# Performance work log

Hardware: AMD Instinct MI355X
Metric: run time of the kernel (lower is better)

The kernel has to match this reference:

```python
import jax, jax.numpy as jnp
import numpy as np

DIM = 1024
BLOCK = 64
N_BLOCKS = DIM // BLOCK
N = 65536
INIT_SCALE = 0.01


def setup_inputs() -> dict:
    key = jax.random.key(0)
    k1, k2 = jax.random.split(key)
    x = jax.random.normal(k1, (N, DIM), dtype=jnp.float32)
    skew_params = jax.random.normal(k2, (N_BLOCKS, BLOCK, BLOCK), dtype=jnp.float32) * INIT_SCALE
    perm = jnp.asarray(np.random.default_rng(0).permutation(DIM), dtype=jnp.int64)
    return {"x": x, "skew_params": skew_params, "perm": perm}


def reference(x, skew_params, perm):
    # Skew-symmetrize each block: A = P - P^T, shape [K, b, b]
    A = skew_params - jnp.swapaxes(skew_params, -1, -2)
    # Per-block orthogonal matrices via matrix exponential, [K, b, b]
    B = jax.vmap(jax.scipy.linalg.expm)(A)
    # Block-diagonal matmul without materializing the dense [dim, dim] matrix:
    # x @ block_diag(B_0..B_{K-1}) == batched per-block matmul on reshaped x.
    xb = x.reshape(x.shape[0], N_BLOCKS, BLOCK)          # [N, K, b]
    yb = jnp.einsum("nkb,kbc->nkc", xb, B)               # [N, K, b]
    y = yb.reshape(x.shape[0], DIM)                      # [N, dim]
    # Shuffle: column permutation
    return y[:, perm]
```

## Files before the change

kernel.cpp:

```cpp
#include <hip/hip_runtime.h>

#define DIM           1024
#define BLK           64
#define NB            16
#define RT            16
#define MAIN_THREADS  1024
#define NWG           256
#define TPW           16
#define P68           68
#define BFRAG_STRIDE  512

typedef float  f32x4  __attribute__((ext_vector_type(4)));
typedef unsigned uintx2 __attribute__((ext_vector_type(2)));
typedef short  bf16x8 __attribute__((ext_vector_type(8)));

static __device__ __forceinline__ ushort f2bf(float f) {
    union { float f; unsigned u; } v; v.f = f;
    unsigned r = v.u + 0x7fffu + ((v.u >> 16) & 1u);
    return (ushort)(r >> 16);
}
static __device__ __forceinline__ float bfhi2f(unsigned hi_bits) {
    union { unsigned u; float f; } v; v.u = hi_bits & 0xffff0000u; return v.f;
}
static __device__ __forceinline__ float bflo2f(unsigned lo_bits) {
    union { unsigned u; float f; } v; v.u = lo_bits << 16; return v.f;
}

#define WAITL()   asm volatile("s_waitcnt lgkmcnt(0)" ::: "memory")
#define SBAR()    __builtin_amdgcn_s_barrier()

__global__ __launch_bounds__(512) void expm_kernel(
        const float* __restrict__ skew, ushort* __restrict__ Btl,
        const int* __restrict__ praw, int* __restrict__ pinv) {
    __shared__ float Asm[BLK][P68];
    __shared__ float Tb[2][BLK][P68];
    __shared__ float Rm[BLK][P68];
    const int tid = threadIdx.x;

    if (blockIdx.x == NB) {
        __shared__ int zc;
        if (tid == 0) zc = 0;
        __syncthreads();
        int local = 0;
        for (int i = tid; i < DIM; i += 512)
            if (praw[i] == 0) local++;
        if (local) atomicAdd(&zc, local);
        __syncthreads();
        const bool is64 = (zc > 100);
        const long long* p64 = (const long long*)praw;
        for (int i = tid; i < DIM; i += 512) {
            const int v = is64 ? (int)p64[i] : praw[i];
            pinv[v] = i;
        }
        return;
    }

    const int k = blockIdx.x;
    const float* P = skew + (size_t)k * (BLK * BLK);

    for (int e = tid; e < BLK * BLK; e += 512) {
        const int i = e >> 6, j = e & 63;
        const float a = P[i * BLK + j] - P[j * BLK + i];
        Asm[i][j]   = a;
        Tb[0][i][j] = a;
        Rm[i][j]    = a + (i == j ? 1.0f : 0.0f);
    }
    __syncthreads();

    const int i0 = (tid >> 4) * 2;
    const int j0 = (tid & 15) * 4;

    for (int n = 2; n <= 7; ++n) {
        const float invn = 1.0f / (float)n;
        const float (*Tc)[P68] = Tb[n & 1];
        float       (*Tn)[P68] = Tb[1 - (n & 1)];
        f32x4 acc0 = {0.f, 0.f, 0.f, 0.f}, acc1 = {0.f, 0.f, 0.f, 0.f};
        for (int b = 0; b < BLK; ++b) {
            const f32x4 av = *(const f32x4*)&Asm[b][j0];
            acc0 += Tc[i0][b]     * av;
            acc1 += Tc[i0 + 1][b] * av;
        }
        acc0 *= invn; acc1 *= invn;
        *(f32x4*)&Tn[i0][j0]     = acc0;
        *(f32x4*)&Tn[i0 + 1][j0] = acc1;
        f32x4 r0 = *(const f32x4*)&Rm[i0][j0];     r0 += acc0; *(f32x4*)&Rm[i0][j0]     = r0;
        f32x4 r1 = *(const f32x4*)&Rm[i0 + 1][j0]; r1 += acc1; *(f32x4*)&Rm[i0 + 1][j0] = r1;
        __syncthreads();
    }

    for (int e = tid; e < BLK * BLK; e += 512) {
        const int b = e >> 6, c = e & 63;
        const int n = c >> 4, m = c & 15;
        const int h = b >> 5, g = (b >> 3) & 3, j = b & 7;
        const size_t idx = (size_t)((k * 4 + n) * 2 + h) * BFRAG_STRIDE
                         + g * 128 + m * 8 + j;
        Btl[idx] = (ushort)f2bf(Rm[b][c]);
    }
}

__global__ __launch_bounds__(MAIN_THREADS) void gsl_main_kernel(
        const float* __restrict__ x, const ushort* __restrict__ Btl,
        const int* __restrict__ pinv, float* __restrict__ out) {
    __shared__ ushort ybuf[2][RT * DIM];

    const int tid  = threadIdx.x;
    const int lane = tid & 63;
    const int w    = tid >> 6;
    const int g    = lane >> 4;
    const int m16  = lane & 15;

    bf16x8 bfr[4][2];
#pragma unroll
    for (int n = 0; n < 4; ++n)
#pragma unroll
        for (int h = 0; h < 2; ++h)
            bfr[n][h] = *(const bf16x8*)(Btl +
                (size_t)((w * 4 + n) * 2 + h) * BFRAG_STRIDE + lane * 8);

    int jb[4];
#pragma unroll
    for (int n = 0; n < 4; ++n)
        jb[n] = pinv[w * 64 + n * 16 + m16] * 2;

    const int tile0 = blockIdx.x * TPW;
    const float* xw = x + w * 64 + g * 8;

    const int rp   = w & 7;
    const int hh   = w >> 3;
    const int q32  = lane & 31;
    const int erow = 2 * rp + (lane >> 5);
    const int ecol = hh * 512 + q32 * 4;

    f32x4 a0, a1, a2, a3;
    {
        const float* xp = xw + (size_t)(tile0 * RT + m16) * DIM;
        a0 = *(const f32x4*)(xp);      a1 = *(const f32x4*)(xp + 4);
        a2 = *(const f32x4*)(xp + 32); a3 = *(const f32x4*)(xp + 36);
    }

    for (int it = 0; it < TPW; ++it) {
        char* const yc = (char*)ybuf[it & 1];

        bf16x8 alo, ahi;
        alo[0] = f2bf(a0[0]); alo[1] = f2bf(a0[1]); alo[2] = f2bf(a0[2]); alo[3] = f2bf(a0[3]);
        alo[4] = f2bf(a1[0]); alo[5] = f2bf(a1[1]); alo[6] = f2bf(a1[2]); alo[7] = f2bf(a1[3]);
        ahi[0] = f2bf(a2[0]); ahi[1] = f2bf(a2[1]); ahi[2] = f2bf(a2[2]); ahi[3] = f2bf(a2[3]);
        ahi[4] = f2bf(a3[0]); ahi[5] = f2bf(a3[1]); ahi[6] = f2bf(a3[2]); ahi[7] = f2bf(a3[3]);

        if (it + 1 < TPW) {
            const float* xp = xw + (size_t)((tile0 + it + 1) * RT + m16) * DIM;
            a0 = *(const f32x4*)(xp);      a1 = *(const f32x4*)(xp + 4);
            a2 = *(const f32x4*)(xp + 32); a3 = *(const f32x4*)(xp + 36);
        }

        f32x4 acc[4];
#pragma unroll
        for (int n = 0; n < 4; ++n) acc[n] = (f32x4){0.f, 0.f, 0.f, 0.f};
#pragma unroll
        for (int n = 0; n < 4; ++n)
            acc[n] = __builtin_amdgcn_mfma_f32_16x16x32_bf16(alo, bfr[n][0], acc[n], 0, 0, 0);
#pragma unroll
        for (int n = 0; n < 4; ++n)
            acc[n] = __builtin_amdgcn_mfma_f32_16x16x32_bf16(ahi, bfr[n][1], acc[n], 0, 0, 0);

#pragma unroll
        for (int n = 0; n < 4; ++n)
#pragma unroll
            for (int i = 0; i < 4; ++i)
                *(ushort*)(yc + (4 * g + i) * 2048 + jb[n]) = f2bf(acc[n][i]);

        if (it) {
            const char* yp = (const char*)ybuf[(it & 1) ^ 1] + erow * 2048;
            float* orow = out + (size_t)((tile0 + it - 1) * RT + erow) * DIM;
#pragma unroll
            for (int s = 0; s < 4; ++s) {
                const int e = ecol + s * 128;
                const uintx2 u = *(const uintx2*)(yp + e * 2);
                f32x4 v;
                v[0] = bflo2f(u[0]); v[1] = bfhi2f(u[0]);
                v[2] = bflo2f(u[1]); v[3] = bfhi2f(u[1]);
                *(f32x4*)(orow + e) = v;
            }
        }

        WAITL(); SBAR();
    }

    {
        const char* yp = (const char*)ybuf[(TPW - 1) & 1] + erow * 2048;
        float* orow = out + (size_t)((tile0 + TPW - 1) * RT + erow) * DIM;
#pragma unroll
        for (int s = 0; s < 4; ++s) {
            const int e = ecol + s * 128;
            const uintx2 u = *(const uintx2*)(yp + e * 2);
            f32x4 v;
            v[0] = bflo2f(u[0]); v[1] = bfhi2f(u[0]);
            v[2] = bflo2f(u[1]); v[3] = bfhi2f(u[1]);
            *(f32x4*)(orow + e) = v;
        }
    }
}

extern "C" void kernel_launch(void* const* d_in, const int* in_sizes, int n_in,
                              void* d_out, int out_size, void* d_ws, size_t ws_size,
                              hipStream_t stream) {
    const float* x    = (const float*)d_in[0];
    const float* skew = (const float*)d_in[1];
    const int*   perm = (const int*)d_in[2];
    float* out = (float*)d_out;

    ushort* Btl  = (ushort*)d_ws;
    int*    pinv = (int*)((char*)d_ws + (size_t)NB * BLK * BLK * sizeof(ushort));

    expm_kernel<<<NB + 1, 512, 0, stream>>>(skew, Btl, perm, pinv);
    gsl_main_kernel<<<NWG, MAIN_THREADS, 0, stream>>>(x, Btl, pinv, out);
}
```

Baseline: 134.3 us.

## Process 32-row tiles per iteration and use packed bf16 conversion instruction

```diff
diff --git a/kernel.cpp b/kernel.cpp
--- a/kernel.cpp
+++ b/kernel.cpp
@@ -3,15 +3,16 @@
 #define DIM           1024
 #define BLK           64
 #define NB            16
-#define RT            16
+#define RT            32
 #define MAIN_THREADS  1024
 #define NWG           256
-#define TPW           16
+#define TPW           8
 #define P68           68
 #define BFRAG_STRIDE  512
 
 typedef float  f32x4  __attribute__((ext_vector_type(4)));
 typedef unsigned uintx2 __attribute__((ext_vector_type(2)));
+typedef int    i32x4  __attribute__((ext_vector_type(4)));
 typedef short  bf16x8 __attribute__((ext_vector_type(8)));
 
 static __device__ __forceinline__ ushort f2bf(float f) {
@@ -24,6 +25,11 @@
 }
 static __device__ __forceinline__ float bflo2f(unsigned lo_bits) {
     union { unsigned u; float f; } v; v.u = lo_bits << 16; return v.f;
+}
+static __device__ __forceinline__ unsigned cvt_pk(float lo, float hi) {
+    unsigned r;
+    asm("v_cvt_pk_bf16_f32 %0, %1, %2" : "=v"(r) : "v"(lo), "v"(hi));
+    return r;
 }
 
 #define WAITL()   asm volatile("s_waitcnt lgkmcnt(0)" ::: "memory")
@@ -98,7 +104,7 @@
     }
 }
 
-__global__ __launch_bounds__(MAIN_THREADS) void gsl_main_kernel(
+__global__ __launch_bounds__(MAIN_THREADS, 1) void gsl_main_kernel(
         const float* __restrict__ x, const ushort* __restrict__ Btl,
         const int* __restrict__ pinv, float* __restrict__ out) {
     __shared__ ushort ybuf[2][RT * DIM];
@@ -125,56 +131,87 @@
     const int tile0 = blockIdx.x * TPW;
     const float* xw = x + w * 64 + g * 8;
 
-    const int rp   = w & 7;
-    const int hh   = w >> 3;
     const int q32  = lane & 31;
-    const int erow = 2 * rp + (lane >> 5);
-    const int ecol = hh * 512 + q32 * 4;
-
-    f32x4 a0, a1, a2, a3;
-    {
-        const float* xp = xw + (size_t)(tile0 * RT + m16) * DIM;
-        a0 = *(const f32x4*)(xp);      a1 = *(const f32x4*)(xp + 4);
-        a2 = *(const f32x4*)(xp + 32); a3 = *(const f32x4*)(xp + 36);
+    const int erow = 2 * w + (lane >> 5);
+
+    f32x4 aP[8];
+#pragma unroll
+    for (int h = 0; h < 2; ++h) {
+        const float* xp = xw + (size_t)(tile0 * RT + h * 16 + m16) * DIM;
+        aP[h * 4 + 0] = *(const f32x4*)(xp);
+        aP[h * 4 + 1] = *(const f32x4*)(xp + 4);
+        aP[h * 4 + 2] = *(const f32x4*)(xp + 32);
+        aP[h * 4 + 3] = *(const f32x4*)(xp + 36);
     }
 
     for (int it = 0; it < TPW; ++it) {
         char* const yc = (char*)ybuf[it & 1];
 
-        bf16x8 alo, ahi;
-        alo[0] = f2bf(a0[0]); alo[1] = f2bf(a0[1]); alo[2] = f2bf(a0[2]); alo[3] = f2bf(a0[3]);
-        alo[4] = f2bf(a1[0]); alo[5] = f2bf(a1[1]); alo[6] = f2bf(a1[2]); alo[7] = f2bf(a1[3]);
-        ahi[0] = f2bf(a2[0]); ahi[1] = f2bf(a2[1]); ahi[2] = f2bf(a2[2]); ahi[3] = f2bf(a2[3]);
-        ahi[4] = f2bf(a3[0]); ahi[5] = f2bf(a3[1]); ahi[6] = f2bf(a3[2]); ahi[7] = f2bf(a3[3]);
+        i32x4 pl0, ph0, pl1, ph1;
+        pl0[0] = cvt_pk(aP[0][0], aP[0][1]); pl0[1] = cvt_pk(aP[0][2], aP[0][3]);
+        pl0[2] = cvt_pk(aP[1][0], aP[1][1]); pl0[3] = cvt_pk(aP[1][2], aP[1][3]);
+        ph0[0] = cvt_pk(aP[2][0], aP[2][1]); ph0[1] = cvt_pk(aP[2][2], aP[2][3]);
+        ph0[2] = cvt_pk(aP[3][0], aP[3][1]); ph0[3] = cvt_pk(aP[3][2], aP[3][3]);
+        pl1[0] = cvt_pk(aP[4][0], aP[4][1]); pl1[1] = cvt_pk(aP[4][2], aP[4][3]);
+        pl1[2] = cvt_pk(aP[5][0], aP[5][1]); pl1[3] = cvt_pk(aP[5][2], aP[5][3]);
+        ph1[0] = cvt_pk(aP[6][0], aP[6][1]); ph1[1] = cvt_pk(aP[6][2], aP[6][3]);
+        ph1[2] = cvt_pk(aP[7][0], aP[7][1]); ph1[3] = cvt_pk(aP[7][2], aP[7][3]);
 
         if (it + 1 < TPW) {
-            const float* xp = xw + (size_t)((tile0 + it + 1) * RT + m16) * DIM;
-            a0 = *(const f32x4*)(xp);      a1 = *(const f32x4*)(xp + 4);
-            a2 = *(const f32x4*)(xp + 32); a3 = *(const f32x4*)(xp + 36);
-        }
-
-        f32x4 acc[4];
-#pragma unroll
-        for (int n = 0; n < 4; ++n) acc[n] = (f32x4){0.f, 0.f, 0.f, 0.f};
-#pragma unroll
-        for (int n = 0; n < 4; ++n)
-            acc[n] = __builtin_amdgcn_mfma_f32_16x16x32_bf16(alo, bfr[n][0], acc[n], 0, 0, 0);
-#pragma unroll
-        for (int n = 0; n < 4; ++n)
-            acc[n] = __builtin_amdgcn_mfma_f32_16x16x32_bf16(ahi, bfr[n][1], acc[n], 0, 0, 0);
-
-#pragma unroll
-        for (int n = 0; n < 4; ++n)
-#pragma unroll
-            for (int i = 0; i < 4; ++i)
-                *(ushort*)(yc + (4 * g + i) * 2048 + jb[n]) = f2bf(acc[n][i]);
+#pragma unroll
+            for (int h = 0; h < 2; ++h) {
+                const float* xp = xw + (size_t)((tile0 + it + 1) * RT + h * 16 + m16) * DIM;
+                aP[h * 4 + 0] = *(const f32x4*)(xp);
+                aP[h * 4 + 1] = *(const f32x4*)(xp + 4);
+                aP[h * 4 + 2] = *(const f32x4*)(xp + 32);
+                aP[h * 4 + 3] = *(const f32x4*)(xp + 36);
+            }
+        }
+
+        {
+            const bf16x8 alo = __builtin_bit_cast(bf16x8, pl0);
+            const bf16x8 ahi = __builtin_bit_cast(bf16x8, ph0);
+            f32x4 acc[4];
+#pragma unroll
+            for (int n = 0; n < 4; ++n) acc[n] = (f32x4){0.f, 0.f, 0.f, 0.f};
+#pragma unroll
+            for (int n = 0; n < 4; ++n)
+                acc[n] = __builtin_amdgcn_mfma_f32_16x16x32_bf16(alo, bfr[n][0], acc[n], 0, 0, 0);
+#pragma unroll
+            for (int n = 0; n < 4; ++n)
+                acc[n] = __builtin_amdgcn_mfma_f32_16x16x32_bf16(ahi, bfr[n][1], acc[n], 0, 0, 0);
+#pragma unroll
+            for (int n = 0; n < 4; ++n)
+#pragma unroll
+                for (int i = 0; i < 4; ++i)
+                    *(ushort*)(yc + (4 * g + i) * 2048 + jb[n]) = f2bf(acc[n][i]);
+        }
+
+        {
+            const bf16x8 alo = __builtin_bit_cast(bf16x8, pl1);
+            const bf16x8 ahi = __builtin_bit_cast(bf16x8, ph1);
+            f32x4 acc[4];
+#pragma unroll
+            for (int n = 0; n < 4; ++n) acc[n] = (f32x4){0.f, 0.f, 0.f, 0.f};
+#pragma unroll
+            for (int n = 0; n < 4; ++n)
+                acc[n] = __builtin_amdgcn_mfma_f32_16x16x32_bf16(alo, bfr[n][0], acc[n], 0, 0, 0);
+#pragma unroll
+            for (int n = 0; n < 4; ++n)
+                acc[n] = __builtin_amdgcn_mfma_f32_16x16x32_bf16(ahi, bfr[n][1], acc[n], 0, 0, 0);
+#pragma unroll
+            for (int n = 0; n < 4; ++n)
+#pragma unroll
+                for (int i = 0; i < 4; ++i)
+                    *(ushort*)(yc + (16 + 4 * g + i) * 2048 + jb[n]) = f2bf(acc[n][i]);
+        }
 
         if (it) {
             const char* yp = (const char*)ybuf[(it & 1) ^ 1] + erow * 2048;
             float* orow = out + (size_t)((tile0 + it - 1) * RT + erow) * DIM;
 #pragma unroll
-            for (int s = 0; s < 4; ++s) {
-                const int e = ecol + s * 128;
+            for (int s = 0; s < 8; ++s) {
+                const int e = q32 * 4 + s * 128;
                 const uintx2 u = *(const uintx2*)(yp + e * 2);
                 f32x4 v;
                 v[0] = bflo2f(u[0]); v[1] = bfhi2f(u[0]);
@@ -190,8 +227,8 @@
         const char* yp = (const char*)ybuf[(TPW - 1) & 1] + erow * 2048;
         float* orow = out + (size_t)((tile0 + TPW - 1) * RT + erow) * DIM;
 #pragma unroll
-        for (int s = 0; s < 4; ++s) {
-            const int e = ecol + s * 128;
+        for (int s = 0; s < 8; ++s) {
+            const int e = q32 * 4 + s * 128;
             const uintx2 u = *(const uintx2*)(yp + e * 2);
             f32x4 v;
             v[0] = bflo2f(u[0]); v[1] = bfhi2f(u[0]);
```

Result: slower. 138.9 us (+3.4%).

## Halve workgroup size so each wave handles two column blocks per tile

Applied to the files above, without the earlier changes.

```diff
diff --git a/kernel.cpp b/kernel.cpp
--- a/kernel.cpp
+++ b/kernel.cpp
@@ -4,14 +4,15 @@
 #define BLK           64
 #define NB            16
 #define RT            16
-#define MAIN_THREADS  1024
-#define NWG           256
-#define TPW           16
+#define MAIN_THREADS  512
+#define NWG           512
+#define TPW           8
 #define P68           68
 #define BFRAG_STRIDE  512
 
 typedef float  f32x4  __attribute__((ext_vector_type(4)));
 typedef unsigned uintx2 __attribute__((ext_vector_type(2)));
+typedef int    i32x4  __attribute__((ext_vector_type(4)));
 typedef short  bf16x8 __attribute__((ext_vector_type(8)));
 
 static __device__ __forceinline__ ushort f2bf(float f) {
@@ -24,6 +25,11 @@
 }
 static __device__ __forceinline__ float bflo2f(unsigned lo_bits) {
     union { unsigned u; float f; } v; v.u = lo_bits << 16; return v.f;
+}
+static __device__ __forceinline__ unsigned cvt_pk(float lo, float hi) {
+    unsigned r;
+    asm("v_cvt_pk_bf16_f32 %0, %1, %2" : "=v"(r) : "v"(lo), "v"(hi));
+    return r;
 }
 
 #define WAITL()   asm volatile("s_waitcnt lgkmcnt(0)" ::: "memory")
@@ -109,72 +115,75 @@
     const int g    = lane >> 4;
     const int m16  = lane & 15;
 
-    bf16x8 bfr[4][2];
-#pragma unroll
-    for (int n = 0; n < 4; ++n)
-#pragma unroll
-        for (int h = 0; h < 2; ++h)
-            bfr[n][h] = *(const bf16x8*)(Btl +
-                (size_t)((w * 4 + n) * 2 + h) * BFRAG_STRIDE + lane * 8);
-
-    int jb[4];
-#pragma unroll
-    for (int n = 0; n < 4; ++n)
-        jb[n] = pinv[w * 64 + n * 16 + m16] * 2;
-
     const int tile0 = blockIdx.x * TPW;
-    const float* xw = x + w * 64 + g * 8;
-
-    const int rp   = w & 7;
-    const int hh   = w >> 3;
+
     const int q32  = lane & 31;
-    const int erow = 2 * rp + (lane >> 5);
-    const int ecol = hh * 512 + q32 * 4;
-
-    f32x4 a0, a1, a2, a3;
+    const int erow = 2 * w + (lane >> 5);
+
+    f32x4 aP0, aP1, aP2, aP3;
     {
-        const float* xp = xw + (size_t)(tile0 * RT + m16) * DIM;
-        a0 = *(const f32x4*)(xp);      a1 = *(const f32x4*)(xp + 4);
-        a2 = *(const f32x4*)(xp + 32); a3 = *(const f32x4*)(xp + 36);
+        const float* xp = x + (size_t)(tile0 * RT + m16) * DIM + w * 64 + g * 8;
+        aP0 = *(const f32x4*)(xp);      aP1 = *(const f32x4*)(xp + 4);
+        aP2 = *(const f32x4*)(xp + 32); aP3 = *(const f32x4*)(xp + 36);
     }
 
     for (int it = 0; it < TPW; ++it) {
         char* const yc = (char*)ybuf[it & 1];
 
-        bf16x8 alo, ahi;
-        alo[0] = f2bf(a0[0]); alo[1] = f2bf(a0[1]); alo[2] = f2bf(a0[2]); alo[3] = f2bf(a0[3]);
-        alo[4] = f2bf(a1[0]); alo[5] = f2bf(a1[1]); alo[6] = f2bf(a1[2]); alo[7] = f2bf(a1[3]);
-        ahi[0] = f2bf(a2[0]); ahi[1] = f2bf(a2[1]); ahi[2] = f2bf(a2[2]); ahi[3] = f2bf(a2[3]);
-        ahi[4] = f2bf(a3[0]); ahi[5] = f2bf(a3[1]); ahi[6] = f2bf(a3[2]); ahi[7] = f2bf(a3[3]);
-
-        if (it + 1 < TPW) {
-            const float* xp = xw + (size_t)((tile0 + it + 1) * RT + m16) * DIM;
-            a0 = *(const f32x4*)(xp);      a1 = *(const f32x4*)(xp + 4);
-            a2 = *(const f32x4*)(xp + 32); a3 = *(const f32x4*)(xp + 36);
-        }
-
-        f32x4 acc[4];
-#pragma unroll
-        for (int n = 0; n < 4; ++n) acc[n] = (f32x4){0.f, 0.f, 0.f, 0.f};
-#pragma unroll
-        for (int n = 0; n < 4; ++n)
-            acc[n] = __builtin_amdgcn_mfma_f32_16x16x32_bf16(alo, bfr[n][0], acc[n], 0, 0, 0);
-#pragma unroll
-        for (int n = 0; n < 4; ++n)
-            acc[n] = __builtin_amdgcn_mfma_f32_16x16x32_bf16(ahi, bfr[n][1], acc[n], 0, 0, 0);
-
-#pragma unroll
-        for (int n = 0; n < 4; ++n)
-#pragma unroll
-            for (int i = 0; i < 4; ++i)
-                *(ushort*)(yc + (4 * g + i) * 2048 + jb[n]) = f2bf(acc[n][i]);
+        for (int bs = 0; bs < 2; ++bs) {
+            const int k = w + 8 * bs;
+
+            bf16x8 bfr[4][2];
+#pragma unroll
+            for (int n = 0; n < 4; ++n)
+#pragma unroll
+                for (int h = 0; h < 2; ++h)
+                    bfr[n][h] = *(const bf16x8*)(Btl +
+                        (size_t)((k * 4 + n) * 2 + h) * BFRAG_STRIDE + lane * 8);
+            int jb[4];
+#pragma unroll
+            for (int n = 0; n < 4; ++n)
+                jb[n] = pinv[k * 64 + n * 16 + m16] * 2;
+
+            i32x4 plo, phi;
+            plo[0] = cvt_pk(aP0[0], aP0[1]); plo[1] = cvt_pk(aP0[2], aP0[3]);
+            plo[2] = cvt_pk(aP1[0], aP1[1]); plo[3] = cvt_pk(aP1[2], aP1[3]);
+            phi[0] = cvt_pk(aP2[0], aP2[1]); phi[1] = cvt_pk(aP2[2], aP2[3]);
+            phi[2] = cvt_pk(aP3[0], aP3[1]); phi[3] = cvt_pk(aP3[2], aP3[3]);
+
+            const int nit = (bs == 0) ? it : it + 1;
+            if (bs == 0 || it + 1 < TPW) {
+                const float* xp = x + (size_t)((tile0 + nit) * RT + m16) * DIM
+                                + (w + 8 * (1 - bs)) * 64 + g * 8;
+                aP0 = *(const f32x4*)(xp);      aP1 = *(const f32x4*)(xp + 4);
+                aP2 = *(const f32x4*)(xp + 32); aP3 = *(const f32x4*)(xp + 36);
+            }
+
+            const bf16x8 alo = __builtin_bit_cast(bf16x8, plo);
+            const bf16x8 ahi = __builtin_bit_cast(bf16x8, phi);
+            f32x4 acc[4];
+#pragma unroll
+            for (int n = 0; n < 4; ++n) acc[n] = (f32x4){0.f, 0.f, 0.f, 0.f};
+#pragma unroll
+            for (int n = 0; n < 4; ++n)
+                acc[n] = __builtin_amdgcn_mfma_f32_16x16x32_bf16(alo, bfr[n][0], acc[n], 0, 0, 0);
+#pragma unroll
+            for (int n = 0; n < 4; ++n)
+                acc[n] = __builtin_amdgcn_mfma_f32_16x16x32_bf16(ahi, bfr[n][1], acc[n], 0, 0, 0);
+
+#pragma unroll
+            for (int n = 0; n < 4; ++n)
+#pragma unroll
+                for (int i = 0; i < 4; ++i)
+                    *(ushort*)(yc + (4 * g + i) * 2048 + jb[n]) = f2bf(acc[n][i]);
+        }
 
         if (it) {
             const char* yp = (const char*)ybuf[(it & 1) ^ 1] + erow * 2048;
             float* orow = out + (size_t)((tile0 + it - 1) * RT + erow) * DIM;
 #pragma unroll
-            for (int s = 0; s < 4; ++s) {
-                const int e = ecol + s * 128;
+            for (int s = 0; s < 8; ++s) {
+                const int e = q32 * 4 + s * 128;
                 const uintx2 u = *(const uintx2*)(yp + e * 2);
                 f32x4 v;
                 v[0] = bflo2f(u[0]); v[1] = bfhi2f(u[0]);
@@ -190,8 +199,8 @@
         const char* yp = (const char*)ybuf[(TPW - 1) & 1] + erow * 2048;
         float* orow = out + (size_t)((tile0 + TPW - 1) * RT + erow) * DIM;
 #pragma unroll
-        for (int s = 0; s < 4; ++s) {
-            const int e = ecol + s * 128;
+        for (int s = 0; s < 8; ++s) {
+            const int e = q32 * 4 + s * 128;
             const uintx2 u = *(const uintx2*)(yp + e * 2);
             f32x4 v;
             v[0] = bflo2f(u[0]); v[1] = bfhi2f(u[0]);
```

New measurement: 138.6 us. 3.2% more time.
